# Kernel optimization log

Measured on AMD Instinct MI355X. Metric: run time of the kernel, lower is better.

The kernel has to match this reference:

```python
import jax, jax.numpy as jnp
import numpy as np

HIDDEN = 2048
NUM_HEADS = 16
HEAD_DIM = 128
WINDOW = 256
BATCH = 2
SEQ = 2048
ROPE_BASE = 10000.0


def apply_rope(t):
    # t: [b, h, s, d]; half-split (rotate-half) rotary embedding
    d = t.shape[-1]
    s = t.shape[-2]
    inv_freq = 1.0 / (ROPE_BASE ** (jnp.arange(0, d, 2, dtype=jnp.float32) / d))  # [d/2]
    freqs = jnp.arange(s, dtype=jnp.float32)[:, None] * inv_freq[None, :]          # [s, d/2]
    cos, sin = jnp.cos(freqs), jnp.sin(freqs)
    t1, t2 = t[..., : d // 2], t[..., d // 2 :]
    return jnp.concatenate([t1 * cos - t2 * sin, t1 * sin + t2 * cos], axis=-1)


def setup_inputs() -> dict:
    key = jax.random.key(0)
    ks = jax.random.split(key, 10)
    dm = HEAD_DIM * NUM_HEADS
    lin_std = 1.0 / np.sqrt(HIDDEN)
    out_std = 1.0 / np.sqrt(dm)
    return {
        "x": jax.random.normal(ks[0], (BATCH, SEQ, HIDDEN), dtype=jnp.float32),
        "W_Q": jax.random.uniform(ks[1], (HIDDEN, dm), jnp.float32, -lin_std, lin_std),
        "b_Q": jax.random.uniform(ks[2], (dm,), jnp.float32, -lin_std, lin_std),
        "W_K": jax.random.uniform(ks[3], (HIDDEN, dm), jnp.float32, -lin_std, lin_std),
        "b_K": jax.random.uniform(ks[4], (dm,), jnp.float32, -lin_std, lin_std),
        "W_V": jax.random.uniform(ks[5], (HIDDEN, dm), jnp.float32, -lin_std, lin_std),
        "b_V": jax.random.uniform(ks[6], (dm,), jnp.float32, -lin_std, lin_std),
        "W_O": jax.random.uniform(ks[7], (dm, HIDDEN), jnp.float32, -out_std, out_std),
        "b_O": jax.random.uniform(ks[8], (HIDDEN,), jnp.float32, -out_std, out_std),
        "key_weights": jax.random.normal(ks[9], (NUM_HEADS,), dtype=jnp.float32),
    }


def reference(x, W_Q, b_Q, W_K, b_K, W_V, b_V, W_O, b_O, key_weights):
    b, s, _ = x.shape
    scale = HEAD_DIM ** -0.5

    def split_heads(t):  # [b, s, h*d] -> [b, h, s, d]
        return t.reshape(b, s, NUM_HEADS, HEAD_DIM).transpose(0, 2, 1, 3)

    q = split_heads(x @ W_Q + b_Q)
    k = split_heads(x @ W_K + b_K)
    v = split_heads(x @ W_V + b_V)

    q = apply_rope(q)
    k = apply_rope(k)

    # num_kv_heads == num_heads here, so group_size == 1: plain per-head attention
    scores = jnp.einsum("bhqd,bhkd->bhqk", q, k) * scale
    scores = scores * key_weights[None, :, None, None]

    # sliding-window causal mask: allow 0 <= i - j <= WINDOW
    i = jnp.arange(s)[:, None]
    j = jnp.arange(s)[None, :]
    allowed = (j <= i) & (j >= i - WINDOW)
    scores = jnp.where(allowed[None, None], scores, -jnp.inf)

    attn = jax.nn.softmax(scores, axis=-1)
    out = jnp.einsum("bhqk,bhkd->bhqd", attn, v)  # [b, h, s, d]
    out = out.transpose(0, 2, 1, 3).reshape(b, s, NUM_HEADS * HEAD_DIM)
    return out @ W_O + b_O
```

## Files before the change

### kernel.cpp

```cpp
#include <hip/hip_runtime.h>
#include <cstdint>

#define SEQn   2048
#define NHn    16
#define HDn    128
#define DMn    2048
#define HIDn   2048
#define BATCHn 2
#define WINn   256
#define MROWS  (BATCHn*SEQn)
#define WELEMS ((size_t)HIDn * DMn)

typedef short s16x8 __attribute__((ext_vector_type(8)));
typedef float f32x4 __attribute__((ext_vector_type(4)));

__device__ __forceinline__ float bf2f(ushort x) {
    union { uint u; float f; } v; v.u = ((uint)x) << 16; return v.f;
}
__device__ __forceinline__ ushort f2bf(float f) {
    union { float f; uint u; } v; v.f = f;
    uint u = v.u;
    return (ushort)((u + 0x7FFFu + ((u >> 16) & 1u)) >> 16);
}

#define GLOAD_LDS16(g, l) __builtin_amdgcn_global_load_lds(                   \
    (const __attribute__((address_space(1))) unsigned int*)(g),               \
    (__attribute__((address_space(3))) unsigned int*)(l), 16, 0, 0)

#define FENCE() do { asm volatile("" ::: "memory");                           \
                     __builtin_amdgcn_sched_barrier(0); } while (0)

__global__ __launch_bounds__(256)
void transpose_all_kernel(const float* __restrict__ WQ, const float* __restrict__ WK,
                          const float* __restrict__ WV, const float* __restrict__ WO,
                          ushort* __restrict__ WT,
                          const float* __restrict__ x, ushort* __restrict__ xb)
{
    const int tid = threadIdx.y * 32 + threadIdx.x;
    if (blockIdx.z == 4) {
        const int bid = blockIdx.y * 32 + blockIdx.x;
        const size_t b0 = (size_t)bid * 8192;
        #pragma unroll
        for (int i = 0; i < 4; ++i) {
            const size_t base = b0 + i * 2048 + tid * 8;
            const float4 a0 = *reinterpret_cast<const float4*>(x + base);
            const float4 a1 = *reinterpret_cast<const float4*>(x + base + 4);
            ushort4 o0, o1;
            o0.x = f2bf(a0.x); o0.y = f2bf(a0.y); o0.z = f2bf(a0.z); o0.w = f2bf(a0.w);
            o1.x = f2bf(a1.x); o1.y = f2bf(a1.y); o1.z = f2bf(a1.z); o1.w = f2bf(a1.w);
            *reinterpret_cast<ushort4*>(xb + base)     = o0;
            *reinterpret_cast<ushort4*>(xb + base + 4) = o1;
        }
        return;
    }
    __shared__ ushort t[64][72];
    const float* src = (blockIdx.z == 0) ? WQ : (blockIdx.z == 1) ? WK
                     : (blockIdx.z == 2) ? WV : WO;
    ushort* dst = WT + (size_t)blockIdx.z * WELEMS;
    const int n0 = blockIdx.x * 64;
    const int k0 = blockIdx.y * 64;
    const int c  = tid & 63;
    const int rr = tid >> 6;
    #pragma unroll
    for (int i = 0; i < 16; ++i) {
        const int r = i * 4 + rr;
        t[c][r] = f2bf(src[(size_t)(k0 + r) * 2048 + n0 + c]);
    }
    __syncthreads();
    const int rowg = tid >> 4;
    const int kc   = (tid & 15) * 4;
    #pragma unroll
    for (int rr2 = 0; rr2 < 4; ++rr2) {
        const int arow = rowg + rr2 * 16;
        const ushort4 v = *reinterpret_cast<const ushort4*>(&t[arow][kc]);
        *reinterpret_cast<ushort4*>(dst + (size_t)(n0 + arow) * 2048 + k0 + kc) = v;
    }
}

__global__ __launch_bounds__(256)
void transpose_cvt_kernel(const float* __restrict__ src, ushort* __restrict__ dst)
{
    __shared__ ushort t[32][33];
    const int tx = threadIdx.x, ty = threadIdx.y;
    const int n  = blockIdx.x * 32 + tx;
    const int k0 = blockIdx.y * 32;
    #pragma unroll
    for (int r = ty; r < 32; r += 8)
        t[r][tx] = f2bf(src[(size_t)(k0 + r) * 2048 + n]);
    __syncthreads();
    const int k  = k0 + tx;
    const int nb = blockIdx.x * 32;
    #pragma unroll
    for (int r = ty; r < 32; r += 8)
        dst[(size_t)(nb + r) * 2048 + k] = t[tx][r];
}

template<int ABF16>
__global__ __launch_bounds__(256)
void gemm_qkv_kernel(const void* __restrict__ Araw, const ushort* __restrict__ WT,
                     const float* __restrict__ bQ, const float* __restrict__ bK,
                     const float* __restrict__ bV,
                     ushort* __restrict__ Qb, ushort* __restrict__ Kb,
                     ushort* __restrict__ Vt)
{
    __shared__ __align__(16) ushort smem[32768];
    const int tid = threadIdx.x;
    const int lin = blockIdx.y * 48 + blockIdx.x;
    const int swz = (lin & 7) * 192 + (lin >> 3);
    const int m0  = (swz / 48) * 128;
    const int n0g = (swz % 48) * 128;
    const int sel = n0g >> 11;
    const int n0  = n0g & 2047;
    const ushort* BT  = WT + (size_t)sel * WELEMS;
    const float* bias = (sel == 0) ? bQ : (sel == 1) ? bK : bV;
    const int w  = tid >> 6;
    const int l  = tid & 63;
    const int wy = w >> 1, wx = w & 1;
    const int q  = l >> 4, lm = l & 15;
    const int sw = lm & 7;

    f32x4 acc[4][4];
    #pragma unroll
    for (int i = 0; i < 4; ++i)
        #pragma unroll
        for (int j = 0; j < 4; ++j) acc[i][j] = (f32x4)0.0f;

    auto stage = [&](int slot, int kt) {
        ushort* AsS = smem + slot * 16384;
        ushort* BsS = AsS + 8192;
        if (ABF16) {
            #pragma unroll
            for (int it = 0; it < 4; ++it) {
                const int v = it * 256 + tid;
                const int r = v >> 3;
                const int cs = ((v & 7) ^ (r & 7)) << 3;
                const ushort* gA = (const ushort*)Araw + (size_t)(m0 + r) * HIDn + kt + cs;
                const ushort* gB = BT + (size_t)(n0 + r) * HIDn + kt + cs;
                GLOAD_LDS16(gA, AsS + (it * 256 + w * 64) * 8);
                GLOAD_LDS16(gB, BsS + (it * 256 + w * 64) * 8);
            }
        } else {
            #pragma unroll
            for (int it = 0; it < 4; ++it) {
                const int v = it * 256 + tid;
                const int r = v >> 3;
                const int c = (v & 7) << 3;
                const float* Af = (const float*)Araw + (size_t)(m0 + r) * HIDn + kt + c;
                const float4 a0 = *reinterpret_cast<const float4*>(Af);
                const float4 a1 = *reinterpret_cast<const float4*>(Af + 4);
                ushort* d = &AsS[(size_t)(v ^ (r & 7)) * 8];
                d[0] = f2bf(a0.x); d[1] = f2bf(a0.y); d[2] = f2bf(a0.z); d[3] = f2bf(a0.w);
                d[4] = f2bf(a1.x); d[5] = f2bf(a1.y); d[6] = f2bf(a1.z); d[7] = f2bf(a1.w);
                const int cs = ((v & 7) ^ (r & 7)) << 3;
                const ushort* gB = BT + (size_t)(n0 + r) * HIDn + kt + cs;
                GLOAD_LDS16(gB, BsS + (it * 256 + w * 64) * 8);
            }
        }
    };

    auto compute = [&](int slot) {
        const ushort* AsS = smem + slot * 16384;
        const ushort* BsS = AsS + 8192;
        #pragma unroll
        for (int ks = 0; ks < 2; ++ks) {
            s16x8 af[4], bfv[4];
            #pragma unroll
            for (int im = 0; im < 4; ++im) {
                const int arow = wy * 64 + im * 16 + lm;
                af[im] = *reinterpret_cast<const s16x8*>(
                    &AsS[arow * 64 + (((ks * 4 + q) ^ sw) << 3)]);
            }
            #pragma unroll
            for (int in = 0; in < 4; ++in) {
                const int brow = wx * 64 + in * 16 + lm;
                bfv[in] = *reinterpret_cast<const s16x8*>(
                    &BsS[brow * 64 + (((ks * 4 + q) ^ sw) << 3)]);
            }
            __builtin_amdgcn_s_setprio(1);
            #pragma unroll
            for (int im = 0; im < 4; ++im)
                #pragma unroll
                for (int in = 0; in < 4; ++in)
                    acc[im][in] = __builtin_amdgcn_mfma_f32_16x16x32_bf16(af[im], bfv[in], acc[im][in], 0, 0, 0);
            __builtin_amdgcn_s_setprio(0);
        }
    };

    const int NT = HIDn / 64;
    stage(0, 0);
    int cur = 0;
    for (int t = 0; t < NT - 1; ++t) {
        stage(cur ^ 1, (t + 1) * 64);
        if (ABF16) asm volatile("s_waitcnt vmcnt(8)" ::: "memory");
        else       asm volatile("s_waitcnt vmcnt(4)" ::: "memory");
        __builtin_amdgcn_s_barrier();
        FENCE();
        compute(cur);
        FENCE();
        if (!ABF16) asm volatile("s_waitcnt lgkmcnt(0)" ::: "memory");
        __builtin_amdgcn_s_barrier();
        FENCE();
        cur ^= 1;
    }
    asm volatile("s_waitcnt vmcnt(0)" ::: "memory");
    __builtin_amdgcn_s_barrier();
    FENCE();
    compute(cur);
    __syncthreads();

    if (sel == 2) {
        ushort* ctile = smem;
        #pragma unroll
        for (int in = 0; in < 4; ++in) {
            const int col = wx * 64 + in * 16 + lm;
            const float bv = bias[n0 + col];
            #pragma unroll
            for (int im = 0; im < 4; ++im) {
                const int row0 = wy * 64 + im * 16 + q * 4;
                #pragma unroll
                for (int r = 0; r < 4; ++r)
                    ctile[col * 136 + row0 + r] = f2bf(acc[im][in][r] + bv);
            }
        }
        __syncthreads();
        const int hh = n0 >> 7;
        const int bb = m0 >> 11;
        const int s0 = m0 & (SEQn - 1);
        const int st = (tid & 15) * 8;
        const int d0 = tid >> 4;
        #pragma unroll
        for (int db = 0; db < 8; ++db) {
            const int d = d0 + db * 16;
            const ushort4 v0 = *reinterpret_cast<const ushort4*>(&ctile[d * 136 + st]);
            const ushort4 v1 = *reinterpret_cast<const ushort4*>(&ctile[d * 136 + st + 4]);
            ushort* dstp = Vt + (((size_t)(bb * NHn + hh)) * HDn + d) * SEQn + s0 + st;
            *reinterpret_cast<ushort4*>(dstp)     = v0;
            *reinterpret_cast<ushort4*>(dstp + 4) = v1;
        }
    } else {
        ushort* ctile = smem;
        #pragma unroll
        for (int in = 0; in < 4; ++in) {
            const int col = wx * 64 + in * 16 + lm;
            const float bv = bias[n0 + col];
            #pragma unroll
            for (int im = 0; im < 4; ++im) {
                const int row0 = wy * 64 + im * 16 + q * 4;
                #pragma unroll
                for (int r = 0; r < 4; ++r)
                    ctile[(row0 + r) * 136 + col] = f2bf(acc[im][in][r] + bv);
            }
        }
        __syncthreads();
        ushort* dst = (sel == 0) ? Qb : Kb;
        const int d = tid & 63;
        const float invf = exp2f(-(float)d * 0.20762050593046f);
        for (int r = tid >> 6; r < 128; r += 4) {
            const int s = (m0 + r) & (SEQn - 1);
            const float ang = (float)s * invf;
            float sn, cs;
            __sincosf(ang, &sn, &cs);
            const float t1 = bf2f(ctile[r * 136 + d]);
            const float t2 = bf2f(ctile[r * 136 + 64 + d]);
            const size_t base = (size_t)(m0 + r) * DMn + n0 + d;
            dst[base]      = f2bf(t1 * cs - t2 * sn);
            dst[base + 64] = f2bf(t1 * sn + t2 * cs);
        }
    }
}

__global__ __launch_bounds__(256)
void gemm_out_kernel(const ushort* __restrict__ A, const ushort* __restrict__ BT,
                     const float* __restrict__ bias, float* __restrict__ C)
{
    __shared__ __align__(16) ushort smem[32768];
    const int tid = threadIdx.x;
    const int lin = blockIdx.y * 16 + blockIdx.x;
    const int swz = (lin & 7) * 64 + (lin >> 3);
    const int m0 = (swz >> 4) * 128;
    const int n0 = (swz & 15) * 128;
    const int w  = tid >> 6;
    const int l  = tid & 63;
    const int wy = w >> 1, wx = w & 1;
    const int q  = l >> 4, lm = l & 15;
    const int sw = lm & 7;

    f32x4 acc[4][4];
    #pragma unroll
    for (int i = 0; i < 4; ++i)
        #pragma unroll
        for (int j = 0; j < 4; ++j) acc[i][j] = (f32x4)0.0f;

    auto stage = [&](int slot, int kt) {
        ushort* AsS = smem + slot * 16384;
        ushort* BsS = AsS + 8192;
        #pragma unroll
        for (int it = 0; it < 4; ++it) {
            const int v = it * 256 + tid;
            const int r = v >> 3;
            const int cs = ((v & 7) ^ (r & 7)) << 3;
            GLOAD_LDS16(A  + (size_t)(m0 + r) * DMn + kt + cs,
                        AsS + (it * 256 + w * 64) * 8);
            GLOAD_LDS16(BT + (size_t)(n0 + r) * DMn + kt + cs,
                        BsS + (it * 256 + w * 64) * 8);
        }
    };

    auto compute = [&](int slot) {
        const ushort* AsS = smem + slot * 16384;
        const ushort* BsS = AsS + 8192;
        #pragma unroll
        for (int ks = 0; ks < 2; ++ks) {
            s16x8 af[4], bfv[4];
            #pragma unroll
            for (int im = 0; im < 4; ++im) {
                const int arow = wy * 64 + im * 16 + lm;
                af[im] = *reinterpret_cast<const s16x8*>(
                    &AsS[arow * 64 + (((ks * 4 + q) ^ sw) << 3)]);
            }
            #pragma unroll
            for (int in = 0; in < 4; ++in) {
                const int brow = wx * 64 + in * 16 + lm;
                bfv[in] = *reinterpret_cast<const s16x8*>(
                    &BsS[brow * 64 + (((ks * 4 + q) ^ sw) << 3)]);
            }
            __builtin_amdgcn_s_setprio(1);
            #pragma unroll
            for (int im = 0; im < 4; ++im)
                #pragma unroll
                for (int in = 0; in < 4; ++in)
                    acc[im][in] = __builtin_amdgcn_mfma_f32_16x16x32_bf16(af[im], bfv[in], acc[im][in], 0, 0, 0);
            __builtin_amdgcn_s_setprio(0);
        }
    };

    const int NT = DMn / 64;
    stage(0, 0);
    int cur = 0;
    for (int t = 0; t < NT - 1; ++t) {
        stage(cur ^ 1, (t + 1) * 64);
        asm volatile("s_waitcnt vmcnt(8)" ::: "memory");
        __builtin_amdgcn_s_barrier();
        FENCE();
        compute(cur);
        FENCE();
        __builtin_amdgcn_s_barrier();
        FENCE();
        cur ^= 1;
    }
    asm volatile("s_waitcnt vmcnt(0)" ::: "memory");
    __builtin_amdgcn_s_barrier();
    FENCE();
    compute(cur);

    #pragma unroll
    for (int in = 0; in < 4; ++in) {
        const int gcol = n0 + wx * 64 + in * 16 + lm;
        const float bv = bias[gcol];
        #pragma unroll
        for (int im = 0; im < 4; ++im) {
            const int grow0 = m0 + wy * 64 + im * 16 + q * 4;
            #pragma unroll
            for (int r = 0; r < 4; ++r)
                C[(size_t)(grow0 + r) * HIDn + gcol] = acc[im][in][r] + bv;
        }
    }
}

__global__ __launch_bounds__(256)
void attn_mfma_kernel(const ushort* Q, const ushort* __restrict__ K,
                      const ushort* __restrict__ Vt, const float* __restrict__ kw,
                      ushort* AO)
{
    __shared__ ushort plds[4][16 * 40];
    const int w  = threadIdx.x >> 6;
    const int l  = threadIdx.x & 63;
    const int q  = l >> 4, lm = l & 15;
    const int bid = blockIdx.x;
    const int swzb = (bid & 7) * 128 + (bid >> 3);
    const int gw = swzb * 4 + w;
    const int qt = gw & 127;
    const int h  = (gw >> 7) & (NHn - 1);
    const int b  = gw >> 11;
    const int q0 = qt * 16;
    const float f = kw[h] * 0.08838834764831845f;

    s16x8 qf[4];
    const size_t qbase = ((size_t)(b * SEQn + q0 + lm)) * DMn + h * HDn;
    #pragma unroll
    for (int ks = 0; ks < 4; ++ks)
        qf[ks] = *reinterpret_cast<const s16x8*>(Q + qbase + ks * 32 + q * 8);

    f32x4 O[8];
    #pragma unroll
    for (int nt = 0; nt < 8; ++nt) O[nt] = (f32x4)0.0f;
    float m[4]    = {-1e30f, -1e30f, -1e30f, -1e30f};
    float lsum[4] = {0.f, 0.f, 0.f, 0.f};

    const int lo = q0 - WINn;
    const int c0 = lo > 0 ? (lo & ~31) : 0;
    const int nch = (q0 + 16 - c0 + 31) >> 5;

    const size_t kbh = ((size_t)(b * SEQn)) * DMn + h * HDn;
    const size_t vbh = ((size_t)(b * NHn + h)) * HDn * SEQn;

    for (int c = 0; c < nch; ++c) {
        const int kc = c0 + c * 32;
        s16x8 vf[8];
        #pragma unroll
        for (int nt = 0; nt < 8; ++nt)
            vf[nt] = *reinterpret_cast<const s16x8*>(
                Vt + vbh + (size_t)(nt * 16 + lm) * SEQn + kc + q * 8);
        f32x4 S[2];
        #pragma unroll
        for (int t = 0; t < 2; ++t) {
            f32x4 acc = (f32x4)0.0f;
            const size_t krow = kbh + (size_t)(kc + t * 16 + lm) * DMn;
            s16x8 kf[4];
            #pragma unroll
            for (int ks = 0; ks < 4; ++ks)
                kf[ks] = *reinterpret_cast<const s16x8*>(K + krow + ks * 32 + q * 8);
            __builtin_amdgcn_s_setprio(1);
            #pragma unroll
            for (int ks = 0; ks < 4; ++ks)
                acc = __builtin_amdgcn_mfma_f32_16x16x32_bf16(qf[ks], kf[ks], acc, 0, 0, 0);
            __builtin_amdgcn_s_setprio(0);
            S[t] = acc;
        }
        const int j0 = kc + lm, j1 = kc + 16 + lm;
        #pragma unroll
        for (int r = 0; r < 4; ++r) {
            const int i = q0 + q * 4 + r;
            float v0 = S[0][r] * f;
            float v1 = S[1][r] * f;
            if (j0 > i || j0 < i - WINn) v0 = -1e30f;
            if (j1 > i || j1 < i - WINn) v1 = -1e30f;
            float mx = fmaxf(v0, v1);
            #pragma unroll
            for (int off = 8; off > 0; off >>= 1)
                mx = fmaxf(mx, __shfl_xor(mx, off));
            const float mn = fmaxf(m[r], mx);
            const float alpha = __expf(m[r] - mn);
            m[r] = mn;
            const ushort h0 = f2bf(__expf(v0 - mn));
            const ushort h1 = f2bf(__expf(v1 - mn));
            plds[w][(q * 4 + r) * 40 + lm]      = h0;
            plds[w][(q * 4 + r) * 40 + 16 + lm] = h1;
            float ps = bf2f(h0) + bf2f(h1);
            #pragma unroll
            for (int off = 8; off > 0; off >>= 1)
                ps += __shfl_xor(ps, off);
            lsum[r] = lsum[r] * alpha + ps;
            #pragma unroll
            for (int nt = 0; nt < 8; ++nt) O[nt][r] *= alpha;
        }
        const s16x8 pf = *reinterpret_cast<const s16x8*>(&plds[w][lm * 40 + q * 8]);
        __builtin_amdgcn_s_setprio(1);
        #pragma unroll
        for (int nt = 0; nt < 8; ++nt)
            O[nt] = __builtin_amdgcn_mfma_f32_16x16x32_bf16(pf, vf[nt], O[nt], 0, 0, 0);
        __builtin_amdgcn_s_setprio(0);
    }
    #pragma unroll
    for (int r = 0; r < 4; ++r) {
        const float inv = 1.0f / lsum[r];
        const size_t orow = ((size_t)(b * SEQn + q0 + q * 4 + r)) * DMn + h * HDn;
        #pragma unroll
        for (int nt = 0; nt < 8; ++nt)
            AO[orow + nt * 16 + lm] = f2bf(O[nt][r] * inv);
    }
}

extern "C" void kernel_launch(void* const* d_in, const int* in_sizes, int n_in,
                              void* d_out, int out_size, void* d_ws, size_t ws_size,
                              hipStream_t stream)
{
    (void)in_sizes; (void)n_in; (void)out_size;
    const float* x  = (const float*)d_in[0];
    const float* WQ = (const float*)d_in[1];
    const float* bQ = (const float*)d_in[2];
    const float* WK = (const float*)d_in[3];
    const float* bK = (const float*)d_in[4];
    const float* WV = (const float*)d_in[5];
    const float* bV = (const float*)d_in[6];
    const float* WO = (const float*)d_in[7];
    const float* bO = (const float*)d_in[8];
    const float* kw = (const float*)d_in[9];
    float* out = (float*)d_out;

    char* ws = (char*)d_ws;
    const size_t AELEMS = (size_t)MROWS * DMn;
    ushort* Qb = (ushort*)ws;
    ushort* Kb = (ushort*)(ws + AELEMS * 2);
    ushort* Vt = (ushort*)(ws + AELEMS * 4);
    ushort* WT = (ushort*)(ws + AELEMS * 6);
    const size_t FULL = AELEMS * 6 + WELEMS * 8 + AELEMS * 2;
    const bool have_full = ws_size >= FULL;
    ushort* xb = (ushort*)(ws + AELEMS * 6 + WELEMS * 8);

    const dim3 tblk(32, 8);

    if (have_full) {
        transpose_all_kernel<<<dim3(32, 32, 5), tblk, 0, stream>>>(WQ, WK, WV, WO, WT, x, xb);
        gemm_qkv_kernel<1><<<dim3(3 * DMn / 128, MROWS / 128), 256, 0, stream>>>(
            xb, WT, bQ, bK, bV, Qb, Kb, Vt);
        attn_mfma_kernel<<<dim3(BATCHn * NHn * (SEQn / 16) / 4), 256, 0, stream>>>(Qb, Kb, Vt, kw, Qb);
        gemm_out_kernel<<<dim3(HIDn / 128, MROWS / 128), 256, 0, stream>>>(
            Qb, WT + 3 * WELEMS, bO, out);
    } else {
        transpose_all_kernel<<<dim3(32, 32, 3), tblk, 0, stream>>>(WQ, WK, WV, WO, WT, x, xb);
        gemm_qkv_kernel<0><<<dim3(3 * DMn / 128, MROWS / 128), 256, 0, stream>>>(
            x, WT, bQ, bK, bV, Qb, Kb, Vt);
        attn_mfma_kernel<<<dim3(BATCHn * NHn * (SEQn / 16) / 4), 256, 0, stream>>>(Qb, Kb, Vt, kw, Qb);
        transpose_cvt_kernel<<<dim3(64, 64), tblk, 0, stream>>>(WO, WT);
        gemm_out_kernel<<<dim3(HIDn / 128, MROWS / 128), 256, 0, stream>>>(Qb, WT, bO, out);
    }
}
```

Before: 381.3 us.

## Process two query tiles per wave in attention and drop GEMM block swizzle

```diff
diff --git a/kernel.cpp b/kernel.cpp
--- a/kernel.cpp
+++ b/kernel.cpp
@@ -105,10 +105,8 @@
 {
     __shared__ __align__(16) ushort smem[32768];
     const int tid = threadIdx.x;
-    const int lin = blockIdx.y * 48 + blockIdx.x;
-    const int swz = (lin & 7) * 192 + (lin >> 3);
-    const int m0  = (swz / 48) * 128;
-    const int n0g = (swz % 48) * 128;
+    const int m0  = blockIdx.y * 128;
+    const int n0g = blockIdx.x * 128;
     const int sel = n0g >> 11;
     const int n0  = n0g & 2047;
     const ushort* BT  = WT + (size_t)sel * WELEMS;
@@ -275,10 +273,8 @@
 {
     __shared__ __align__(16) ushort smem[32768];
     const int tid = threadIdx.x;
-    const int lin = blockIdx.y * 16 + blockIdx.x;
-    const int swz = (lin & 7) * 64 + (lin >> 3);
-    const int m0 = (swz >> 4) * 128;
-    const int n0 = (swz & 15) * 128;
+    const int m0 = blockIdx.y * 128;
+    const int n0 = blockIdx.x * 128;
     const int w  = tid >> 6;
     const int l  = tid & 63;
     const int wy = w >> 1, wx = w & 1;
@@ -372,34 +368,38 @@
                       const ushort* __restrict__ Vt, const float* __restrict__ kw,
                       ushort* AO)
 {
-    __shared__ ushort plds[4][16 * 40];
+    __shared__ ushort plds[4][2][16 * 40];
     const int w  = threadIdx.x >> 6;
     const int l  = threadIdx.x & 63;
     const int q  = l >> 4, lm = l & 15;
     const int bid = blockIdx.x;
-    const int swzb = (bid & 7) * 128 + (bid >> 3);
+    const int swzb = (bid & 7) * 64 + (bid >> 3);
     const int gw = swzb * 4 + w;
-    const int qt = gw & 127;
-    const int h  = (gw >> 7) & (NHn - 1);
-    const int b  = gw >> 11;
-    const int q0 = qt * 16;
+    const int qt2 = gw & 63;
+    const int h  = (gw >> 6) & (NHn - 1);
+    const int b  = gw >> 10;
+    const int q0 = qt2 * 32;
     const float f = kw[h] * 0.08838834764831845f;
 
-    s16x8 qf[4];
-    const size_t qbase = ((size_t)(b * SEQn + q0 + lm)) * DMn + h * HDn;
-    #pragma unroll
-    for (int ks = 0; ks < 4; ++ks)
-        qf[ks] = *reinterpret_cast<const s16x8*>(Q + qbase + ks * 32 + q * 8);
-
-    f32x4 O[8];
-    #pragma unroll
-    for (int nt = 0; nt < 8; ++nt) O[nt] = (f32x4)0.0f;
-    float m[4]    = {-1e30f, -1e30f, -1e30f, -1e30f};
-    float lsum[4] = {0.f, 0.f, 0.f, 0.f};
+    s16x8 qfA[4], qfB[4];
+    const size_t qbaseA = ((size_t)(b * SEQn + q0 + lm)) * DMn + h * HDn;
+    const size_t qbaseB = qbaseA + (size_t)16 * DMn;
+    #pragma unroll
+    for (int ks = 0; ks < 4; ++ks) {
+        qfA[ks] = *reinterpret_cast<const s16x8*>(Q + qbaseA + ks * 32 + q * 8);
+        qfB[ks] = *reinterpret_cast<const s16x8*>(Q + qbaseB + ks * 32 + q * 8);
+    }
+
+    f32x4 OA[8], OB[8];
+    #pragma unroll
+    for (int nt = 0; nt < 8; ++nt) { OA[nt] = (f32x4)0.0f; OB[nt] = (f32x4)0.0f; }
+    float mA[4], mB[4], lA[4], lB[4];
+    #pragma unroll
+    for (int r = 0; r < 4; ++r) { mA[r] = -1e30f; mB[r] = -1e30f; lA[r] = 0.f; lB[r] = 0.f; }
 
     const int lo = q0 - WINn;
-    const int c0 = lo > 0 ? (lo & ~31) : 0;
-    const int nch = (q0 + 16 - c0 + 31) >> 5;
+    const int c0 = lo > 0 ? lo : 0;
+    const int nch = (q0 + 32 - c0) >> 5;
 
     const size_t kbh = ((size_t)(b * SEQn)) * DMn + h * HDn;
     const size_t vbh = ((size_t)(b * NHn + h)) * HDn * SEQn;
@@ -411,10 +411,10 @@
         for (int nt = 0; nt < 8; ++nt)
             vf[nt] = *reinterpret_cast<const s16x8*>(
                 Vt + vbh + (size_t)(nt * 16 + lm) * SEQn + kc + q * 8);
-        f32x4 S[2];
+        f32x4 SA[2], SB[2];
         #pragma unroll
         for (int t = 0; t < 2; ++t) {
-            f32x4 acc = (f32x4)0.0f;
+            f32x4 aA = (f32x4)0.0f, aB = (f32x4)0.0f;
             const size_t krow = kbh + (size_t)(kc + t * 16 + lm) * DMn;
             s16x8 kf[4];
             #pragma unroll
@@ -422,52 +422,88 @@
                 kf[ks] = *reinterpret_cast<const s16x8*>(K + krow + ks * 32 + q * 8);
             __builtin_amdgcn_s_setprio(1);
             #pragma unroll
-            for (int ks = 0; ks < 4; ++ks)
-                acc = __builtin_amdgcn_mfma_f32_16x16x32_bf16(qf[ks], kf[ks], acc, 0, 0, 0);
+            for (int ks = 0; ks < 4; ++ks) {
+                aA = __builtin_amdgcn_mfma_f32_16x16x32_bf16(qfA[ks], kf[ks], aA, 0, 0, 0);
+                aB = __builtin_amdgcn_mfma_f32_16x16x32_bf16(qfB[ks], kf[ks], aB, 0, 0, 0);
+            }
             __builtin_amdgcn_s_setprio(0);
-            S[t] = acc;
+            SA[t] = aA; SB[t] = aB;
         }
         const int j0 = kc + lm, j1 = kc + 16 + lm;
         #pragma unroll
         for (int r = 0; r < 4; ++r) {
-            const int i = q0 + q * 4 + r;
-            float v0 = S[0][r] * f;
-            float v1 = S[1][r] * f;
-            if (j0 > i || j0 < i - WINn) v0 = -1e30f;
-            if (j1 > i || j1 < i - WINn) v1 = -1e30f;
-            float mx = fmaxf(v0, v1);
-            #pragma unroll
-            for (int off = 8; off > 0; off >>= 1)
-                mx = fmaxf(mx, __shfl_xor(mx, off));
-            const float mn = fmaxf(m[r], mx);
-            const float alpha = __expf(m[r] - mn);
-            m[r] = mn;
-            const ushort h0 = f2bf(__expf(v0 - mn));
-            const ushort h1 = f2bf(__expf(v1 - mn));
-            plds[w][(q * 4 + r) * 40 + lm]      = h0;
-            plds[w][(q * 4 + r) * 40 + 16 + lm] = h1;
-            float ps = bf2f(h0) + bf2f(h1);
-            #pragma unroll
-            for (int off = 8; off > 0; off >>= 1)
-                ps += __shfl_xor(ps, off);
-            lsum[r] = lsum[r] * alpha + ps;
-            #pragma unroll
-            for (int nt = 0; nt < 8; ++nt) O[nt][r] *= alpha;
-        }
-        const s16x8 pf = *reinterpret_cast<const s16x8*>(&plds[w][lm * 40 + q * 8]);
+            {
+                const int i = q0 + q * 4 + r;
+                float v0 = SA[0][r] * f;
+                float v1 = SA[1][r] * f;
+                if (j0 > i || j0 < i - WINn) v0 = -1e30f;
+                if (j1 > i || j1 < i - WINn) v1 = -1e30f;
+                float mx = fmaxf(v0, v1);
+                #pragma unroll
+                for (int off = 8; off > 0; off >>= 1)
+                    mx = fmaxf(mx, __shfl_xor(mx, off));
+                const float mn = fmaxf(mA[r], mx);
+                const float alpha = __expf(mA[r] - mn);
+                mA[r] = mn;
+                const ushort h0 = f2bf(__expf(v0 - mn));
+                const ushort h1 = f2bf(__expf(v1 - mn));
+                plds[w][0][(q * 4 + r) * 40 + lm]      = h0;
+                plds[w][0][(q * 4 + r) * 40 + 16 + lm] = h1;
+                float ps = bf2f(h0) + bf2f(h1);
+                #pragma unroll
+                for (int off = 8; off > 0; off >>= 1)
+                    ps += __shfl_xor(ps, off);
+                lA[r] = lA[r] * alpha + ps;
+                #pragma unroll
+                for (int nt = 0; nt < 8; ++nt) OA[nt][r] *= alpha;
+            }
+            {
+                const int i = q0 + 16 + q * 4 + r;
+                float v0 = SB[0][r] * f;
+                float v1 = SB[1][r] * f;
+                if (j0 > i || j0 < i - WINn) v0 = -1e30f;
+                if (j1 > i || j1 < i - WINn) v1 = -1e30f;
+                float mx = fmaxf(v0, v1);
+                #pragma unroll
+                for (int off = 8; off > 0; off >>= 1)
+                    mx = fmaxf(mx, __shfl_xor(mx, off));
+                const float mn = fmaxf(mB[r], mx);
+                const float alpha = __expf(mB[r] - mn);
+                mB[r] = mn;
+                const ushort h0 = f2bf(__expf(v0 - mn));
+                const ushort h1 = f2bf(__expf(v1 - mn));
+                plds[w][1][(q * 4 + r) * 40 + lm]      = h0;
+                plds[w][1][(q * 4 + r) * 40 + 16 + lm] = h1;
+                float ps = bf2f(h0) + bf2f(h1);
+                #pragma unroll
+                for (int off = 8; off > 0; off >>= 1)
+                    ps += __shfl_xor(ps, off);
+                lB[r] = lB[r] * alpha + ps;
+                #pragma unroll
+                for (int nt = 0; nt < 8; ++nt) OB[nt][r] *= alpha;
+            }
+        }
+        const s16x8 pfA = *reinterpret_cast<const s16x8*>(&plds[w][0][lm * 40 + q * 8]);
+        const s16x8 pfB = *reinterpret_cast<const s16x8*>(&plds[w][1][lm * 40 + q * 8]);
         __builtin_amdgcn_s_setprio(1);
         #pragma unroll
-        for (int nt = 0; nt < 8; ++nt)
-            O[nt] = __builtin_amdgcn_mfma_f32_16x16x32_bf16(pf, vf[nt], O[nt], 0, 0, 0);
+        for (int nt = 0; nt < 8; ++nt) {
+            OA[nt] = __builtin_amdgcn_mfma_f32_16x16x32_bf16(pfA, vf[nt], OA[nt], 0, 0, 0);
+            OB[nt] = __builtin_amdgcn_mfma_f32_16x16x32_bf16(pfB, vf[nt], OB[nt], 0, 0, 0);
+        }
         __builtin_amdgcn_s_setprio(0);
     }
     #pragma unroll
     for (int r = 0; r < 4; ++r) {
-        const float inv = 1.0f / lsum[r];
-        const size_t orow = ((size_t)(b * SEQn + q0 + q * 4 + r)) * DMn + h * HDn;
-        #pragma unroll
-        for (int nt = 0; nt < 8; ++nt)
-            AO[orow + nt * 16 + lm] = f2bf(O[nt][r] * inv);
+        const float invA = 1.0f / lA[r];
+        const float invB = 1.0f / lB[r];
+        const size_t orowA = ((size_t)(b * SEQn + q0 + q * 4 + r)) * DMn + h * HDn;
+        const size_t orowB = orowA + (size_t)16 * DMn;
+        #pragma unroll
+        for (int nt = 0; nt < 8; ++nt) {
+            AO[orowA + nt * 16 + lm] = f2bf(OA[nt][r] * invA);
+            AO[orowB + nt * 16 + lm] = f2bf(OB[nt][r] * invB);
+        }
     }
 }
 
@@ -499,19 +535,20 @@
     ushort* xb = (ushort*)(ws + AELEMS * 6 + WELEMS * 8);
 
     const dim3 tblk(32, 8);
+    const int attn_grid = BATCHn * NHn * (SEQn / 32) / 4;
 
     if (have_full) {
         transpose_all_kernel<<<dim3(32, 32, 5), tblk, 0, stream>>>(WQ, WK, WV, WO, WT, x, xb);
         gemm_qkv_kernel<1><<<dim3(3 * DMn / 128, MROWS / 128), 256, 0, stream>>>(
             xb, WT, bQ, bK, bV, Qb, Kb, Vt);
-        attn_mfma_kernel<<<dim3(BATCHn * NHn * (SEQn / 16) / 4), 256, 0, stream>>>(Qb, Kb, Vt, kw, Qb);
+        attn_mfma_kernel<<<dim3(attn_grid), 256, 0, stream>>>(Qb, Kb, Vt, kw, Qb);
         gemm_out_kernel<<<dim3(HIDn / 128, MROWS / 128), 256, 0, stream>>>(
             Qb, WT + 3 * WELEMS, bO, out);
     } else {
         transpose_all_kernel<<<dim3(32, 32, 3), tblk, 0, stream>>>(WQ, WK, WV, WO, WT, x, xb);
         gemm_qkv_kernel<0><<<dim3(3 * DMn / 128, MROWS / 128), 256, 0, stream>>>(
             x, WT, bQ, bK, bV, Qb, Kb, Vt);
-        attn_mfma_kernel<<<dim3(BATCHn * NHn * (SEQn / 16) / 4), 256, 0, stream>>>(Qb, Kb, Vt, kw, Qb);
+        attn_mfma_kernel<<<dim3(attn_grid), 256, 0, stream>>>(Qb, Kb, Vt, kw, Qb);
         transpose_cvt_kernel<<<dim3(64, 64), tblk, 0, stream>>>(WO, WT);
         gemm_out_kernel<<<dim3(HIDn / 128, MROWS / 128), 256, 0, stream>>>(Qb, WT, bO, out);
     }
```

After: 365.9 us. 1.04x faster.
